# Kernel tuning notes

Hardware: AMD Instinct MI355X
Metric: run time of the kernel (lower is better)

Reference implementation:

```python
import jax, jax.numpy as jnp
import numpy as np

NUM_HEADS = 16
EMBED_DIM = 1024
BSZ, T, S = 8, 1024, 1024
NEG_INF = -1e30


def setup_inputs() -> dict:
    key = jax.random.key(0)
    ks = jax.random.split(key, 12)
    E = EMBED_DIM
    decoder_state = jax.random.normal(ks[0], (BSZ, T, E), dtype=jnp.float32)
    source_hids = jax.random.normal(ks[1], (S, BSZ, E), dtype=jnp.float32)
    # realistic padding mask: True = padded position (masked out)
    lengths = jax.random.randint(ks[2], (BSZ,), S // 2, S + 1)
    src_len_mask = jnp.arange(S)[None, :] >= lengths[:, None]  # (BSZ, S) bool
    init = 1.0 / np.sqrt(E)
    Wq = jax.random.uniform(ks[3], (E, E), minval=-init, maxval=init)
    bq = jax.random.uniform(ks[4], (E,), minval=-init, maxval=init)
    Wk = jax.random.uniform(ks[5], (E, E), minval=-init, maxval=init)
    bk = jax.random.uniform(ks[6], (E,), minval=-init, maxval=init)
    Wv = jax.random.uniform(ks[7], (E, E), minval=-init, maxval=init)
    bv = jax.random.uniform(ks[8], (E,), minval=-init, maxval=init)
    Wo = jax.random.uniform(ks[9], (E, E), minval=-init, maxval=init)
    bo = jax.random.uniform(ks[10], (E,), minval=-init, maxval=init)
    return {"decoder_state": decoder_state, "source_hids": source_hids,
            "src_len_mask": src_len_mask, "Wq": Wq, "bq": bq, "Wk": Wk,
            "bk": bk, "Wv": Wv, "bv": bv, "Wo": Wo, "bo": bo}


def reference(decoder_state, source_hids, src_len_mask, Wq, bq, Wk, bk, Wv, bv, Wo, bo):
    B, Tq, E = decoder_state.shape
    Sk = source_hids.shape[0]
    H = NUM_HEADS
    hd = E // H
    scaling = hd ** (-0.5)

    query = jnp.swapaxes(decoder_state, 0, 1)  # (T, B, E)
    q = (query @ Wq.T + bq) * scaling          # (T, B, E)
    k = source_hids @ Wk.T + bk                # (S, B, E)
    v = source_hids @ Wv.T + bv                # (S, B, E)

    q = q.reshape(Tq, B, H, hd)
    k = k.reshape(Sk, B, H, hd)
    v = v.reshape(Sk, B, H, hd)

    scores = jnp.einsum("tbhd,sbhd->bhts", q, k)  # (B, H, T, S)
    scores = jnp.where(src_len_mask[:, None, None, :], NEG_INF, scores)
    weights = jax.nn.softmax(scores, axis=-1)     # (B, H, T, S); dropout p=0

    attn = jnp.einsum("bhts,sbhd->tbhd", weights, v).reshape(Tq, B, E)
    attn = attn @ Wo.T + bo                       # (T, B, E)

    # need_weights: mean over heads -> (B, T, S); then transpose(0,2) -> (S, T, B)
    attn_weights_out = jnp.swapaxes(weights.mean(axis=1), 0, 2)
    # squeeze=True is a no-op here since T != 1
    return attn, attn_weights_out
```

## Files before the change

### kernel.cpp

```cpp
#include <hip/hip_runtime.h>
#include <stdint.h>
#include <stddef.h>

typedef __attribute__((ext_vector_type(8))) short bf16x8;
typedef __attribute__((ext_vector_type(4))) float f32x4;
typedef __attribute__((ext_vector_type(4))) uint32_t u32x4;

#define DEVINL static __device__ __forceinline__

DEVINL float b2f(uint16_t u) {
  uint32_t x = ((uint32_t)u) << 16;
  float f;
  __builtin_memcpy(&f, &x, 4);
  return f;
}

DEVINL uint16_t f2b(float f) {
  uint32_t u;
  __builtin_memcpy(&u, &f, 4);
  return (uint16_t)((u + 0x7fffu + ((u >> 16) & 1u)) >> 16);
}

DEVINL void gload16(const void* gsrc, void* ldst) {
  __builtin_amdgcn_global_load_lds(
      (const __attribute__((address_space(1))) void*)gsrc,
      (__attribute__((address_space(3))) void*)ldst, 16, 0, 0);
}

__global__ void detect_kernel(const void* __restrict__ wq, const void* __restrict__ mask,
                              const void* __restrict__ bq, const void* __restrict__ bk,
                              const void* __restrict__ bv, const void* __restrict__ bo,
                              int* __restrict__ hdr, float* __restrict__ bias) {
  __shared__ int sflag, smask32, slen[8];
  const int tid = threadIdx.x;
  if (tid == 0) { sflag = 0; smask32 = 0; }
  if (tid < 8) slen[tid] = 0;
  __syncthreads();
  const uint16_t* w16 = (const uint16_t*)wq;
  int f = 0;
  for (int i = tid; i < 4096; i += 256) {
    uint16_t u = w16[i];
    uint32_t e = (u >> 7) & 0xFFu;
    if (fabsf(b2f(u)) > 0.25f || e == 0xFFu) f = 1;
  }
  if (f) atomicOr(&sflag, 1);
  const uint8_t* mb = (const uint8_t*)mask;
  int m32 = 0;
  for (int i = tid; i < 8191; i += 256) {
    if ((i & 1023) != 1023 && mb[i] != 0 && mb[i + 1] == 0) m32 = 1;
  }
  if (m32) atomicOr(&smask32, 1);
  __syncthreads();
  if (smask32) {
    const int* mi = (const int*)mask;
    for (int i = tid; i < 8192; i += 256) { if (mi[i] == 0) atomicAdd(&slen[i >> 10], 1); }
  } else {
    for (int i = tid; i < 8192; i += 256) { if (mb[i] == 0) atomicAdd(&slen[i >> 10], 1); }
  }
  __syncthreads();
  if (tid == 0) hdr[0] = sflag;
  if (tid < 8) hdr[1 + tid] = slen[tid];
  const void* bs[4] = {bq, bk, bv, bo};
  for (int j = 0; j < 4; ++j) {
    for (int i = tid; i < 1024; i += 256) {
      float v = sflag ? ((const float*)bs[j])[i] : b2f(((const uint16_t*)bs[j])[i]);
      bias[j * 1024 + i] = v;
    }
  }
}

__global__ __launch_bounds__(256)
void convert_kernel(const void* __restrict__ s0, const void* __restrict__ s1,
                    const void* __restrict__ s2, const void* __restrict__ s3,
                    const void* __restrict__ s4, const void* __restrict__ s5,
                    uint16_t* __restrict__ d0, uint16_t* __restrict__ d1,
                    uint16_t* __restrict__ d2, const int* __restrict__ hdr, int doW) {
  const int isf = hdr[0];
  const size_t n01 = 1048576;
  const size_t nw = 131072;
  const size_t total = doW ? (2 * n01 + 4 * nw) : (2 * n01);
  size_t gid = (size_t)blockIdx.x * 256 + threadIdx.x;
  const size_t stride = (size_t)gridDim.x * 256;
  for (; gid < total; gid += stride) {
    const void* sp;
    uint16_t* dp;
    size_t off;
    if (gid < n01) { sp = s0; dp = d0; off = gid; }
    else if (gid < 2 * n01) { sp = s1; dp = d1; off = gid - n01; }
    else {
      const size_t w = (gid - 2 * n01) >> 17;
      off = (gid - 2 * n01) & (nw - 1);
      sp = (w == 0) ? s2 : (w == 1) ? s3 : (w == 2) ? s4 : s5;
      dp = d2 + w * 1048576;
    }
    if (isf) {
      const float* fp = (const float*)sp + off * 8;
      const f32x4 a = *(const f32x4*)fp;
      const f32x4 c = *(const f32x4*)(fp + 4);
      u32x4 r;
      r[0] = (uint32_t)f2b(a[0]) | ((uint32_t)f2b(a[1]) << 16);
      r[1] = (uint32_t)f2b(a[2]) | ((uint32_t)f2b(a[3]) << 16);
      r[2] = (uint32_t)f2b(c[0]) | ((uint32_t)f2b(c[1]) << 16);
      r[3] = (uint32_t)f2b(c[2]) | ((uint32_t)f2b(c[3]) << 16);
      *(u32x4*)(dp + off * 8) = r;
    } else {
      *(u32x4*)(dp + off * 8) = *(const u32x4*)((const uint16_t*)sp + off * 8);
    }
  }
}

enum { MQ = 0, MK = 1, MV = 2, MO = 3 };

DEVINL u32x4 load8w(const void* __restrict__ src, bool f32, size_t eoff) {
  if (!f32) {
    return *(const u32x4*)((const uint16_t*)src + eoff);
  }
  const float* p = (const float*)src + eoff;
  const f32x4 a = *(const f32x4*)p;
  const f32x4 c = *(const f32x4*)(p + 4);
  u32x4 r;
  r[0] = (uint32_t)f2b(a[0]) | ((uint32_t)f2b(a[1]) << 16);
  r[1] = (uint32_t)f2b(a[2]) | ((uint32_t)f2b(a[3]) << 16);
  r[2] = (uint32_t)f2b(c[0]) | ((uint32_t)f2b(c[1]) << 16);
  r[3] = (uint32_t)f2b(c[2]) | ((uint32_t)f2b(c[3]) << 16);
  return r;
}

template <int MODE>
__global__ __launch_bounds__(256)
void gemm_bt(const uint16_t* __restrict__ Ab, const void* __restrict__ Wr,
             const float* __restrict__ bias, const int* __restrict__ hdr,
             void* __restrict__ outp, float scale, int wIsBf16) {
  __shared__ __align__(16) uint16_t lA[8192];
  __shared__ __align__(16) uint16_t lB[8192];
  const int tid = threadIdx.x, lane = tid & 63, wave = tid >> 6;
  const int bm = blockIdx.x, bn = blockIdx.y;
  const int isf = hdr[0];
  const bool wF32 = (wIsBf16 == 0) && (isf != 0);
  const int wm = wave >> 1, wn = wave & 1;
  const int g = lane >> 4, cc = lane & 15;
  const int lr = lane >> 3, lc = lane & 7;
  const int scc = (lc ^ lr) * 8;

  f32x4 acc[4][4];
#pragma unroll
  for (int i = 0; i < 4; ++i)
#pragma unroll
    for (int j = 0; j < 4; ++j) acc[i][j] = (f32x4){0.f, 0.f, 0.f, 0.f};

  for (int kt = 0; kt < 16; ++kt) {
    __syncthreads();
#pragma unroll
    for (int q = 0; q < 4; ++q) {
      const int j = wave * 4 + q;
      gload16(Ab + (size_t)(bm * 128 + j * 8 + lr) * 1024 + kt * 64 + scc, &lA[j * 512]);
    }
    if (!wF32) {
#pragma unroll
      for (int q = 0; q < 4; ++q) {
        const int j = wave * 4 + q;
        gload16((const uint16_t*)Wr + (size_t)(bn * 128 + j * 8 + lr) * 1024 + kt * 64 + scc, &lB[j * 512]);
      }
    } else {
#pragma unroll
      for (int q = 0; q < 4; ++q) {
        const int j = wave * 4 + q;
        const u32x4 rv = load8w(Wr, true, (size_t)(bn * 128 + j * 8 + lr) * 1024 + kt * 64 + lc * 8);
        *(u32x4*)&lB[j * 512 + lr * 64 + ((lc ^ lr) * 8)] = rv;
      }
    }
    __syncthreads();
#pragma unroll
    for (int kk = 0; kk < 2; ++kk) {
      bf16x8 af[4], bfr[4];
#pragma unroll
      for (int mi = 0; mi < 4; ++mi) {
        const int row = wm * 64 + mi * 16 + cc;
        af[mi] = *(const bf16x8*)&lA[row * 64 + (((kk * 4 + g) ^ (cc & 7)) << 3)];
      }
#pragma unroll
      for (int ni = 0; ni < 4; ++ni) {
        const int row = wn * 64 + ni * 16 + cc;
        bfr[ni] = *(const bf16x8*)&lB[row * 64 + (((kk * 4 + g) ^ (cc & 7)) << 3)];
      }
#pragma unroll
      for (int mi = 0; mi < 4; ++mi)
#pragma unroll
        for (int ni = 0; ni < 4; ++ni)
          acc[mi][ni] = __builtin_amdgcn_mfma_f32_16x16x32_bf16(af[mi], bfr[ni], acc[mi][ni], 0, 0, 0);
    }
  }
#pragma unroll
  for (int mi = 0; mi < 4; ++mi) {
#pragma unroll
    for (int ni = 0; ni < 4; ++ni) {
      const int col = bn * 128 + wn * 64 + ni * 16 + cc;
      const float bv = bias[col];
      const int r0 = bm * 128 + wm * 64 + mi * 16 + g * 4;
#pragma unroll
      for (int r = 0; r < 4; ++r) {
        const int row = r0 + r;
        const float v = (acc[mi][ni][r] + bv) * scale;
        if (MODE == MQ) {
          const int b = row >> 10, t = row & 1023, h = col >> 6, d = col & 63;
          ((uint16_t*)outp)[(((size_t)(b * 16 + h) << 10) + t) * 64 + d] = f2b(v);
        } else if (MODE == MK) {
          const int s = row >> 3, b = row & 7, h = col >> 6, d = col & 63;
          ((uint16_t*)outp)[(((size_t)(b * 16 + h) << 10) + s) * 64 + d] = f2b(v);
        } else if (MODE == MV) {
          const int s = row >> 3, b = row & 7, h = col >> 6, d = col & 63;
          ((uint16_t*)outp)[(((size_t)(b * 16 + h) << 6) + d) * 1024 + s] = f2b(v);
        } else {
          const size_t o = (size_t)row * 1024 + col;
          if (isf) ((float*)outp)[o] = v;
          else ((uint16_t*)outp)[o] = f2b(v);
        }
      }
    }
  }
}

__global__ __launch_bounds__(1024)
void attn_kernel(const uint16_t* __restrict__ Qh, const uint16_t* __restrict__ Kh,
                 const uint16_t* __restrict__ Vh, const int* __restrict__ hdr,
                 uint16_t* __restrict__ AP, uint16_t* __restrict__ Wm) {
  __shared__ __align__(16) uint16_t kbuf[2][8192];
  __shared__ __align__(16) uint16_t vbuf[2][8192];
  __shared__ __align__(16) uint16_t pstash[32][1024];
  __shared__ float pvx[2][32][68];

  const int tid = threadIdx.x, lane = tid & 63, w = tid >> 6;
  const int g = lane >> 4, cc = lane & 15;
  const int wt = w >> 3, ws = w & 7;
  const int dq = (w >> 1) & 3, ks = w & 1;
  const int b = blockIdx.x & 7, tt = blockIdx.x >> 3;
  const int t0 = tt * 32;
  const int len = hdr[1 + b];
  const int tme = tid >> 5, s5 = tid & 31;

  auto stage = [&](int p, int buf) {
    const int hh = p >> 3, st = p & 7;
    const uint16_t* Kb = Kh + ((size_t)(b * 16 + hh) << 16);
    const uint16_t* Vt = Vh + ((size_t)(b * 16 + hh) << 16);
    {
      const int row = tid >> 3;
      const int c = (tid & 7) ^ (row & 7);
      gload16(Kb + (st * 128 + row) * 64 + c * 8, &kbuf[buf][w * 512]);
    }
    {
      const int d = tid >> 4;
      const int c = tid & 15;
      const int cg = (c & 8) | ((c ^ (d & 7)) & 7);
      gload16(Vt + d * 1024 + st * 128 + cg * 8, &vbuf[buf][w * 512]);
    }
  };

  stage(0, 0);

  float wmean[32];
#pragma unroll
  for (int j = 0; j < 32; ++j) wmean[j] = 0.f;

  for (int h = 0; h < 16; ++h) {
    const uint16_t* Qb = Qh + ((size_t)(b * 16 + h) << 16) + (((size_t)(t0 + wt * 16 + cc)) << 6);
    const bf16x8 qf0 = *(const bf16x8*)(Qb + g * 8);
    const bf16x8 qf1 = *(const bf16x8*)(Qb + 32 + g * 8);
    f32x4 pv = (f32x4){0.f, 0.f, 0.f, 0.f};
    for (int st = 0; st < 8; ++st) {
      const int p = h * 8 + st;
      const int cur = p & 1;
      asm volatile("s_waitcnt vmcnt(0)" ::: "memory");
      __builtin_amdgcn_sched_barrier(0);
      __builtin_amdgcn_s_barrier();
      if (p + 1 < 128) stage(p + 1, cur ^ 1);
      {
        const int row = ws * 16 + cc;
        f32x4 a = (f32x4){0.f, 0.f, 0.f, 0.f};
#pragma unroll
        for (int kk = 0; kk < 2; ++kk) {
          const bf16x8 kf = *(const bf16x8*)&kbuf[cur][row * 64 + (((kk * 4 + g) ^ (cc & 7)) << 3)];
          a = __builtin_amdgcn_mfma_f32_16x16x32_bf16(kk ? qf1 : qf0, kf, a, 0, 0, 0);
        }
        const int s = st * 128 + row;
        const bool msk = (s >= len);
        const int cbase = st * 16 + ws * 2 + (cc >> 3);
#pragma unroll
        for (int r = 0; r < 4; ++r) {
          const float v = msk ? 0.f : __expf(a[r]);
          const int tl = wt * 16 + g * 4 + r;
          const int cs = (cbase & ~7) | ((cbase ^ tl) & 7);
          pstash[tl][(cs << 3) + (cc & 7)] = f2b(v);
        }
      }
      asm volatile("s_waitcnt lgkmcnt(0)" ::: "memory");
      __builtin_amdgcn_sched_barrier(0);
      __builtin_amdgcn_s_barrier();
      {
        const int tr = wt * 16 + cc;
#pragma unroll
        for (int kk = 0; kk < 2; ++kk) {
          const int ca = st * 16 + ks * 8 + kk * 4 + g;
          const int ca2 = (ca & ~7) | ((ca ^ tr) & 7);
          const bf16x8 af = *(const bf16x8*)&pstash[tr][ca2 << 3];
          const int cv = ks * 8 + kk * 4 + g;
          const int cv2 = (cv & 8) | ((cv ^ (cc & 7)) & 7);
          const bf16x8 vf = *(const bf16x8*)&vbuf[cur][(dq * 16 + cc) * 128 + (cv2 << 3)];
          pv = __builtin_amdgcn_mfma_f32_16x16x32_bf16(af, vf, pv, 0, 0, 0);
        }
      }
    }
#pragma unroll
    for (int r = 0; r < 4; ++r)
      pvx[ks][wt * 16 + g * 4 + r][dq * 16 + cc] = pv[r];
    float winv;
    {
      uint32_t p4[16];
#pragma unroll
      for (int q = 0; q < 4; ++q) {
        const int c = s5 + 32 * q;
        const int c2 = (c & ~7) | ((c ^ tme) & 7);
        *(u32x4*)&p4[q * 4] = *(const u32x4*)&pstash[tme][c2 << 3];
      }
      float sm = 0.f;
#pragma unroll
      for (int j = 0; j < 16; ++j) {
        sm += b2f((uint16_t)(p4[j] & 0xffffu));
        sm += b2f((uint16_t)(p4[j] >> 16));
      }
#pragma unroll
      for (int m = 16; m >= 1; m >>= 1) sm += __shfl_xor(sm, m, 64);
      winv = 1.f / sm;
#pragma unroll
      for (int j = 0; j < 16; ++j) {
        wmean[2 * j] += b2f((uint16_t)(p4[j] & 0xffffu)) * winv;
        wmean[2 * j + 1] += b2f((uint16_t)(p4[j] >> 16)) * winv;
      }
    }
    asm volatile("s_waitcnt lgkmcnt(0)" ::: "memory");
    __builtin_amdgcn_sched_barrier(0);
    __builtin_amdgcn_s_barrier();
    {
      const int d0 = s5 * 2;
      const float v0 = (pvx[0][tme][d0] + pvx[1][tme][d0]) * winv;
      const float v1 = (pvx[0][tme][d0 + 1] + pvx[1][tme][d0 + 1]) * winv;
      const uint32_t pk = (uint32_t)f2b(v0) | ((uint32_t)f2b(v1) << 16);
      *(uint32_t*)(AP + ((((size_t)(t0 + tme)) * 8 + b) << 10) + h * 64 + d0) = pk;
    }
  }

  {
    uint16_t* dst = Wm + (((size_t)(b * 1024 + t0 + tme)) << 10);
#pragma unroll
    for (int q = 0; q < 4; ++q) {
      uint16_t ob[8];
#pragma unroll
      for (int e = 0; e < 8; ++e) ob[e] = f2b(wmean[q * 8 + e] * 0.0625f);
      *(u32x4*)(dst + q * 256 + s5 * 8) = *(const u32x4*)ob;
    }
  }
}

__global__ __launch_bounds__(256)
void wtrans_kernel(const uint16_t* __restrict__ Wm, const int* __restrict__ hdr,
                   void* __restrict__ outBase) {
  __shared__ uint16_t lt[8][32][68];
  const int tid = threadIdx.x;
  const int s0 = blockIdx.x * 64, t0 = blockIdx.y * 32;
  const int isf = hdr[0];
  const int rr = tid >> 4;
  const int sc = (tid & 15) * 4;
#pragma unroll
  for (int p = 0; p < 16; ++p) {
    const int row = p * 16 + rr;
    const int b = row >> 5, t = row & 31;
    const uint64_t v = *(const uint64_t*)(Wm + (((size_t)(b * 1024 + t0 + t)) << 10) + s0 + sc);
    *(uint64_t*)&lt[b][t][sc] = v;
  }
  __syncthreads();
#pragma unroll
  for (int p = 0; p < 8; ++p) {
    const int pair = p * 256 + tid;
    const int t = pair & 31, s = pair >> 5;
    const size_t o = 8388608 + ((size_t)(s0 + s) * 1024 + (t0 + t)) * 8;
    if (isf) {
      f32x4 v0, v1;
#pragma unroll
      for (int b = 0; b < 4; ++b) v0[b] = b2f(lt[b][t][s]);
#pragma unroll
      for (int b = 0; b < 4; ++b) v1[b] = b2f(lt[b + 4][t][s]);
      *(f32x4*)((float*)outBase + o) = v0;
      *(f32x4*)((float*)outBase + o + 4) = v1;
    } else {
      u32x4 v;
#pragma unroll
      for (int q = 0; q < 4; ++q)
        v[q] = (uint32_t)lt[2 * q][t][s] | ((uint32_t)lt[2 * q + 1][t][s] << 16);
      *(u32x4*)((uint16_t*)outBase + o) = v;
    }
  }
}

__global__ void fill_pattern(uint32_t* p, size_t n) {
  size_t i = (size_t)blockIdx.x * 256 + threadIdx.x;
  const size_t stride = (size_t)gridDim.x * 256;
  for (; i < n; i += stride) p[i] = 0x3f3f3f3fu;
}

extern "C" void kernel_launch(void* const* d_in, const int* in_sizes, int n_in,
                              void* d_out, int out_size, void* d_ws, size_t ws_size,
                              hipStream_t stream) {
  char* ws = (char*)d_ws;
  int* hdr = (int*)ws;
  float* bias = (float*)(ws + 4096);
  uint16_t* Q = (uint16_t*)(ws + (1u << 20));
  uint16_t* K = Q + 8388608;
  uint16_t* V = K + 8388608;
  uint16_t* AP = V + 8388608;
  uint16_t* Wm = AP + 8388608;
  uint16_t* dec_b = AP;
  uint16_t* src_b = Wm;
  const size_t needBase = (1ull << 20) + 5ull * 16777216ull;
  const size_t needFull = needBase + 8ull * 1048576ull;
  uint16_t* Wb = (uint16_t*)(ws + needBase);
  const int useConvW = (ws_size >= needFull) ? 1 : 0;
  if (ws_size < needBase) {
    fill_pattern<<<1024, 256, 0, stream>>>((uint32_t*)d_out, (size_t)out_size / 2);
    return;
  }

  detect_kernel<<<1, 256, 0, stream>>>(d_in[3], d_in[2], d_in[4], d_in[6], d_in[8], d_in[10], hdr, bias);

  convert_kernel<<<4096, 256, 0, stream>>>(d_in[0], d_in[1], d_in[3], d_in[5], d_in[7], d_in[9],
                                           dec_b, src_b, Wb, hdr, useConvW);

  const void* Wq = useConvW ? (const void*)(Wb + 0 * 1048576) : (const void*)d_in[3];
  const void* Wk = useConvW ? (const void*)(Wb + 1 * 1048576) : (const void*)d_in[5];
  const void* Wv = useConvW ? (const void*)(Wb + 2 * 1048576) : (const void*)d_in[7];
  const void* Wo = useConvW ? (const void*)(Wb + 3 * 1048576) : (const void*)d_in[9];

  dim3 gg(64, 8);
  gemm_bt<MQ><<<gg, 256, 0, stream>>>(dec_b, Wq, bias, hdr, Q, 0.125f, useConvW);
  gemm_bt<MK><<<gg, 256, 0, stream>>>(src_b, Wk, bias + 1024, hdr, K, 1.f, useConvW);
  gemm_bt<MV><<<gg, 256, 0, stream>>>(src_b, Wv, bias + 2048, hdr, V, 1.f, useConvW);

  attn_kernel<<<256, 1024, 0, stream>>>(Q, K, V, hdr, AP, Wm);

  wtrans_kernel<<<dim3(16, 32), 256, 0, stream>>>(Wm, hdr, d_out);

  gemm_bt<MO><<<gg, 256, 0, stream>>>(AP, Wo, bias + 3072, hdr, d_out, 1.f, useConvW);
}
```

Baseline: 303.4 us.

## Software-pipeline PV matmul one stage behind QK and halve GEMM N-tile

The attention kernel now stages V one step later and computes the P·V product for the previous stage inside the same barrier interval as the current QK^T. This removes one block-wide barrier per stage, and a drain step after the loop handles the last stage. Separately, the projection GEMMs switch to a 128x64 tile with twice as many blocks (grid 64x16), aiming for better CU occupancy at the cost of more A-tile reloads. The pstash and double-buffer reuse across stages carries a correctness risk: the single remaining barrier must order both the pstash writes and the reads of V and K.

```diff
diff --git a/kernel.cpp b/kernel.cpp
--- a/kernel.cpp
+++ b/kernel.cpp
@@ -132,7 +132,7 @@
              const float* __restrict__ bias, const int* __restrict__ hdr,
              void* __restrict__ outp, float scale, int wIsBf16) {
   __shared__ __align__(16) uint16_t lA[8192];
-  __shared__ __align__(16) uint16_t lB[8192];
+  __shared__ __align__(16) uint16_t lB[4096];
   const int tid = threadIdx.x, lane = tid & 63, wave = tid >> 6;
   const int bm = blockIdx.x, bn = blockIdx.y;
   const int isf = hdr[0];
@@ -142,11 +142,11 @@
   const int lr = lane >> 3, lc = lane & 7;
   const int scc = (lc ^ lr) * 8;
 
-  f32x4 acc[4][4];
+  f32x4 acc[4][2];
 #pragma unroll
   for (int i = 0; i < 4; ++i)
 #pragma unroll
-    for (int j = 0; j < 4; ++j) acc[i][j] = (f32x4){0.f, 0.f, 0.f, 0.f};
+    for (int j = 0; j < 2; ++j) acc[i][j] = (f32x4){0.f, 0.f, 0.f, 0.f};
 
   for (int kt = 0; kt < 16; ++kt) {
     __syncthreads();
@@ -157,44 +157,44 @@
     }
     if (!wF32) {
 #pragma unroll
-      for (int q = 0; q < 4; ++q) {
-        const int j = wave * 4 + q;
-        gload16((const uint16_t*)Wr + (size_t)(bn * 128 + j * 8 + lr) * 1024 + kt * 64 + scc, &lB[j * 512]);
+      for (int q = 0; q < 2; ++q) {
+        const int j = wave * 2 + q;
+        gload16((const uint16_t*)Wr + (size_t)(bn * 64 + j * 8 + lr) * 1024 + kt * 64 + scc, &lB[j * 512]);
       }
     } else {
 #pragma unroll
-      for (int q = 0; q < 4; ++q) {
-        const int j = wave * 4 + q;
-        const u32x4 rv = load8w(Wr, true, (size_t)(bn * 128 + j * 8 + lr) * 1024 + kt * 64 + lc * 8);
+      for (int q = 0; q < 2; ++q) {
+        const int j = wave * 2 + q;
+        const u32x4 rv = load8w(Wr, true, (size_t)(bn * 64 + j * 8 + lr) * 1024 + kt * 64 + lc * 8);
         *(u32x4*)&lB[j * 512 + lr * 64 + ((lc ^ lr) * 8)] = rv;
       }
     }
     __syncthreads();
 #pragma unroll
     for (int kk = 0; kk < 2; ++kk) {
-      bf16x8 af[4], bfr[4];
+      bf16x8 af[4], bfr[2];
 #pragma unroll
       for (int mi = 0; mi < 4; ++mi) {
         const int row = wm * 64 + mi * 16 + cc;
         af[mi] = *(const bf16x8*)&lA[row * 64 + (((kk * 4 + g) ^ (cc & 7)) << 3)];
       }
 #pragma unroll
-      for (int ni = 0; ni < 4; ++ni) {
-        const int row = wn * 64 + ni * 16 + cc;
+      for (int ni = 0; ni < 2; ++ni) {
+        const int row = wn * 32 + ni * 16 + cc;
         bfr[ni] = *(const bf16x8*)&lB[row * 64 + (((kk * 4 + g) ^ (cc & 7)) << 3)];
       }
 #pragma unroll
       for (int mi = 0; mi < 4; ++mi)
 #pragma unroll
-        for (int ni = 0; ni < 4; ++ni)
+        for (int ni = 0; ni < 2; ++ni)
           acc[mi][ni] = __builtin_amdgcn_mfma_f32_16x16x32_bf16(af[mi], bfr[ni], acc[mi][ni], 0, 0, 0);
     }
   }
 #pragma unroll
   for (int mi = 0; mi < 4; ++mi) {
 #pragma unroll
-    for (int ni = 0; ni < 4; ++ni) {
-      const int col = bn * 128 + wn * 64 + ni * 16 + cc;
+    for (int ni = 0; ni < 2; ++ni) {
+      const int col = bn * 64 + wn * 32 + ni * 16 + cc;
       const float bv = bias[col];
       const int r0 = bm * 128 + wm * 64 + mi * 16 + g * 4;
 #pragma unroll
@@ -238,24 +238,23 @@
   const int len = hdr[1 + b];
   const int tme = tid >> 5, s5 = tid & 31;
 
-  auto stage = [&](int p, int buf) {
+  auto stageK = [&](int p, int buf) {
     const int hh = p >> 3, st = p & 7;
     const uint16_t* Kb = Kh + ((size_t)(b * 16 + hh) << 16);
+    const int row = tid >> 3;
+    const int c = (tid & 7) ^ (row & 7);
+    gload16(Kb + (st * 128 + row) * 64 + c * 8, &kbuf[buf][w * 512]);
+  };
+  auto stageV = [&](int p, int buf) {
+    const int hh = p >> 3, st = p & 7;
     const uint16_t* Vt = Vh + ((size_t)(b * 16 + hh) << 16);
-    {
-      const int row = tid >> 3;
-      const int c = (tid & 7) ^ (row & 7);
-      gload16(Kb + (st * 128 + row) * 64 + c * 8, &kbuf[buf][w * 512]);
-    }
-    {
-      const int d = tid >> 4;
-      const int c = tid & 15;
-      const int cg = (c & 8) | ((c ^ (d & 7)) & 7);
-      gload16(Vt + d * 1024 + st * 128 + cg * 8, &vbuf[buf][w * 512]);
-    }
+    const int d = tid >> 4;
+    const int c = tid & 15;
+    const int cg = (c & 8) | ((c ^ (d & 7)) & 7);
+    gload16(Vt + d * 1024 + st * 128 + cg * 8, &vbuf[buf][w * 512]);
   };
 
-  stage(0, 0);
+  stageK(0, 0);
 
   float wmean[32];
 #pragma unroll
@@ -268,17 +267,17 @@
     f32x4 pv = (f32x4){0.f, 0.f, 0.f, 0.f};
     for (int st = 0; st < 8; ++st) {
       const int p = h * 8 + st;
-      const int cur = p & 1;
-      asm volatile("s_waitcnt vmcnt(0)" ::: "memory");
+      asm volatile("s_waitcnt vmcnt(0) lgkmcnt(0)" ::: "memory");
       __builtin_amdgcn_sched_barrier(0);
       __builtin_amdgcn_s_barrier();
-      if (p + 1 < 128) stage(p + 1, cur ^ 1);
+      if (p + 1 < 128) stageK(p + 1, (p + 1) & 1);
+      stageV(p, p & 1);
       {
         const int row = ws * 16 + cc;
         f32x4 a = (f32x4){0.f, 0.f, 0.f, 0.f};
 #pragma unroll
         for (int kk = 0; kk < 2; ++kk) {
-          const bf16x8 kf = *(const bf16x8*)&kbuf[cur][row * 64 + (((kk * 4 + g) ^ (cc & 7)) << 3)];
+          const bf16x8 kf = *(const bf16x8*)&kbuf[p & 1][row * 64 + (((kk * 4 + g) ^ (cc & 7)) << 3)];
           a = __builtin_amdgcn_mfma_f32_16x16x32_bf16(kk ? qf1 : qf0, kf, a, 0, 0, 0);
         }
         const int s = st * 128 + row;
@@ -292,21 +291,35 @@
           pstash[tl][(cs << 3) + (cc & 7)] = f2b(v);
         }
       }
-      asm volatile("s_waitcnt lgkmcnt(0)" ::: "memory");
-      __builtin_amdgcn_sched_barrier(0);
-      __builtin_amdgcn_s_barrier();
-      {
+      if (st > 0) {
+        const int stp = st - 1;
         const int tr = wt * 16 + cc;
 #pragma unroll
         for (int kk = 0; kk < 2; ++kk) {
-          const int ca = st * 16 + ks * 8 + kk * 4 + g;
+          const int ca = stp * 16 + ks * 8 + kk * 4 + g;
           const int ca2 = (ca & ~7) | ((ca ^ tr) & 7);
           const bf16x8 af = *(const bf16x8*)&pstash[tr][ca2 << 3];
           const int cv = ks * 8 + kk * 4 + g;
           const int cv2 = (cv & 8) | ((cv ^ (cc & 7)) & 7);
-          const bf16x8 vf = *(const bf16x8*)&vbuf[cur][(dq * 16 + cc) * 128 + (cv2 << 3)];
+          const bf16x8 vf = *(const bf16x8*)&vbuf[stp & 1][(dq * 16 + cc) * 128 + (cv2 << 3)];
           pv = __builtin_amdgcn_mfma_f32_16x16x32_bf16(af, vf, pv, 0, 0, 0);
         }
+      }
+    }
+    asm volatile("s_waitcnt vmcnt(0) lgkmcnt(0)" ::: "memory");
+    __builtin_amdgcn_sched_barrier(0);
+    __builtin_amdgcn_s_barrier();
+    {
+      const int tr = wt * 16 + cc;
+#pragma unroll
+      for (int kk = 0; kk < 2; ++kk) {
+        const int ca = 7 * 16 + ks * 8 + kk * 4 + g;
+        const int ca2 = (ca & ~7) | ((ca ^ tr) & 7);
+        const bf16x8 af = *(const bf16x8*)&pstash[tr][ca2 << 3];
+        const int cv = ks * 8 + kk * 4 + g;
+        const int cv2 = (cv & 8) | ((cv ^ (cc & 7)) & 7);
+        const bf16x8 vf = *(const bf16x8*)&vbuf[1][(dq * 16 + cc) * 128 + (cv2 << 3)];
+        pv = __builtin_amdgcn_mfma_f32_16x16x32_bf16(af, vf, pv, 0, 0, 0);
       }
     }
 #pragma unroll
@@ -438,7 +451,7 @@
   const void* Wv = useConvW ? (const void*)(Wb + 2 * 1048576) : (const void*)d_in[7];
   const void* Wo = useConvW ? (const void*)(Wb + 3 * 1048576) : (const void*)d_in[9];
 
-  dim3 gg(64, 8);
+  dim3 gg(64, 16);
   gemm_bt<MQ><<<gg, 256, 0, stream>>>(dec_b, Wq, bias, hdr, Q, 0.125f, useConvW);
   gemm_bt<MK><<<gg, 256, 0, stream>>>(src_b, Wk, bias + 1024, hdr, K, 1.f, useConvW);
   gemm_bt<MV><<<gg, 256, 0, stream>>>(src_b, Wv, bias + 2048, hdr, V, 1.f, useConvW);
```

After: 382.7 us. +26.1%, slower.
